# Performance work log

Hardware: AMD Instinct MI355X
Metric: run time of the kernel (lower is better)

## Reference

```python
import jax, jax.numpy as jnp
import numpy as np
import math

D_MODEL = 768
H = 12
B = 2
N = 2048


def _layernorm(x, w, b, eps=1e-5):
    mu = jnp.mean(x, axis=-1, keepdims=True)
    var = jnp.var(x, axis=-1, keepdims=True)
    return (x - mu) / jnp.sqrt(var + eps) * w + b


def _mha(q, k, v, h):
    # q,k,v: [B,N,D] -> [B,h,N,dk]
    Bq, Nq, D = q.shape
    dk = D // h
    q = q.reshape(Bq, Nq, h, dk).transpose(0, 2, 1, 3)
    k = k.reshape(Bq, Nq, h, dk).transpose(0, 2, 1, 3)
    v = v.reshape(Bq, Nq, h, dk).transpose(0, 2, 1, 3)
    att = jnp.einsum('bhnd,bhmd->bhnm', q, k) / math.sqrt(dk)
    att = jax.nn.softmax(att, axis=-1)
    out = jnp.einsum('bhnm,bhmd->bhnd', att, v)
    return out.transpose(0, 2, 1, 3).reshape(Bq, Nq, D)


def setup_inputs() -> dict:
    key = jax.random.key(0)
    ks = jax.random.split(key, 12)
    d = D_MODEL
    w = lambda k: jax.random.normal(k, (d, d), jnp.float32) * 0.001
    inp = {
        'rgb': jax.random.normal(ks[0], (B, N, d), jnp.float32),
        'ir': jax.random.normal(ks[1], (B, N, d), jnp.float32),
        'ln0_w': jnp.ones((d,), jnp.float32), 'ln0_b': jnp.zeros((d,), jnp.float32),
        'ln1_w': jnp.ones((d,), jnp.float32), 'ln1_b': jnp.zeros((d,), jnp.float32),
        'Wq_vis': w(ks[2]), 'bq_vis': jnp.zeros((d,), jnp.float32),
        'Wk_vis': w(ks[3]), 'bk_vis': jnp.zeros((d,), jnp.float32),
        'Wq_ir': w(ks[4]), 'bq_ir': jnp.zeros((d,), jnp.float32),
        'Wk_ir': w(ks[5]), 'bk_ir': jnp.zeros((d,), jnp.float32),
        'Wv_vis': w(ks[6]), 'bv_vis': jnp.zeros((d,), jnp.float32),
        'Wv_ir': w(ks[7]), 'bv_ir': jnp.zeros((d,), jnp.float32),
        'Wo_vis': w(ks[8]), 'bo_vis': jnp.zeros((d,), jnp.float32),
        'Wo_ir': w(ks[9]), 'bo_ir': jnp.zeros((d,), jnp.float32),
    }
    return inp


def reference(rgb, ir, ln0_w, ln0_b, ln1_w, ln1_b,
              Wq_vis, bq_vis, Wk_vis, bk_vis, Wq_ir, bq_ir, Wk_ir, bk_ir,
              Wv_vis, bv_vis, Wv_ir, bv_ir, Wo_vis, bo_vis, Wo_ir, bo_ir):
    rgb_n = _layernorm(rgb, ln0_w, ln0_b)
    ir_n = _layernorm(ir, ln1_w, ln1_b)
    q_vis = rgb_n @ Wq_vis + bq_vis
    k_vis = rgb_n @ Wk_vis + bk_vis
    q_ir = ir_n @ Wq_ir + bq_ir
    k_ir = ir_n @ Wk_ir + bk_ir
    v_vis = rgb_n @ Wv_vis + bv_vis
    v_ir = ir_n @ Wv_ir + bv_ir
    out_vis = _mha(q_ir, k_vis, v_vis, H) @ Wo_vis + bo_vis
    out_ir = _mha(q_vis, k_ir, v_ir, H) @ Wo_ir + bo_ir
    return (out_vis, out_ir)
```

## Files before the change

kernel.cpp:

```cpp
#include <hip/hip_runtime.h>
#include <stdint.h>

#define NTOK 4096
#define DM   768

typedef unsigned short u16;
typedef __attribute__((ext_vector_type(8))) short bf16x8;
typedef __attribute__((ext_vector_type(4))) float f32x4;

__device__ __forceinline__ u16 f2bf(float f){
  union { float f; unsigned u; } x; x.f = f;
  return (u16)((x.u + 0x7fffu + ((x.u >> 16) & 1u)) >> 16);
}
__device__ __forceinline__ unsigned fbits(float f){
  union { float f; unsigned u; } x; x.f = f; return x.u;
}
__device__ __forceinline__ int invk(int t){
  return (((t>>3)&1)<<4) | (((t>>2)&1)<<3) | (((t>>4)&1)<<2) | (t&3);
}

__device__ __forceinline__ void dma16(u16* lds, const u16* g){
  __builtin_amdgcn_global_load_lds(
      (const __attribute__((address_space(1))) unsigned*)g,
      (__attribute__((address_space(3))) unsigned*)lds, 16, 0, 0);
}

struct PreArgs {
  const float* wsrc[8]; u16* wdst[8];
  const float* rgb; const float* ir;
  const float* w0; const float* b0; const float* w1; const float* b1;
  u16* rgbn; u16* irn;
};

__global__ __launch_bounds__(256) void k_pre(PreArgs a){
  __shared__ float T[64][65];
  __shared__ float red[8];
  int bid = blockIdx.x;
  int t = threadIdx.x;
  if (bid < 1152){
    int z = bid / 144, r = bid % 144;
    int k0 = (r % 12) * 64, n0 = (r / 12) * 64;
    const float* W = a.wsrc[z];
    u16* Wt = a.wdst[z];
    int rr = t >> 4, c4 = (t & 15) * 4;
    #pragma unroll
    for (int it = 0; it < 4; ++it){
      int row = rr + it * 16;
      float4 v = *(const float4*)(W + (size_t)(k0 + row) * DM + n0 + c4);
      T[row][c4+0] = v.x; T[row][c4+1] = v.y; T[row][c4+2] = v.z; T[row][c4+3] = v.w;
    }
    __syncthreads();
    #pragma unroll
    for (int it = 0; it < 4; ++it){
      int row = rr + it * 16;
      union { u16 us[4]; uint2 u2; } pk;
      #pragma unroll
      for (int i = 0; i < 4; i++) pk.us[i] = f2bf(T[c4+i][row]);
      *(uint2*)(Wt + (size_t)(n0 + row) * DM + k0 + c4) = pk.u2;
    }
  } else {
    int row = bid - 1152;
    const float *src, *w, *b; u16* dst;
    if (row < NTOK){ src = a.rgb + (size_t)row * DM; w = a.w0; b = a.b0; dst = a.rgbn + (size_t)row * DM; }
    else { int r2 = row - NTOK; src = a.ir + (size_t)r2 * DM; w = a.w1; b = a.b1; dst = a.irn + (size_t)r2 * DM; }
    float v0 = src[t], v1 = src[t+256], v2 = src[t+512];
    float s = v0+v1+v2, ss = v0*v0 + v1*v1 + v2*v2;
    #pragma unroll
    for (int m = 1; m < 64; m <<= 1){ s += __shfl_xor(s, m, 64); ss += __shfl_xor(ss, m, 64); }
    int wv = t >> 6;
    if ((t & 63) == 0){ red[wv] = s; red[4+wv] = ss; }
    __syncthreads();
    s  = red[0]+red[1]+red[2]+red[3];
    ss = red[4]+red[5]+red[6]+red[7];
    float mu   = s * (1.f/768.f);
    float var  = ss * (1.f/768.f) - mu*mu;
    float rstd = rsqrtf(var + 1e-5f);
    dst[t]     = f2bf((v0-mu)*rstd*w[t]     + b[t]);
    dst[t+256] = f2bf((v1-mu)*rstd*w[t+256] + b[t+256]);
    dst[t+512] = f2bf((v2-mu)*rstd*w[t+512] + b[t+512]);
  }
}

struct MmArgs { const u16* A[6]; const u16* Bm[6]; const float* bias[6]; void* out[6]; float scale[6]; int mode[6]; };

__global__ __launch_bounds__(256) void k_mm(MmArgs g){
  __shared__ u16 As[2][128*32];
  __shared__ u16 Bs[2][128*32];
  int z = blockIdx.z;
  int mode = g.mode[z];
  const u16* A = g.A[z];
  const u16* B = g.Bm[z];
  const float* bias = g.bias[z];
  float sc = g.scale[z];
  int bx = blockIdx.x;
  int m0, n0;
  if (mode == 2){ m0 = (bx % 6) * 128; n0 = (bx / 6) * 128; }
  else          { m0 = (bx & 31) * 128; n0 = (bx >> 5) * 128; }
  int t = threadIdx.x, lane = t & 63, w = t >> 6, l15 = lane & 15, quad = lane >> 4;
  int wm = (w >> 1) * 64, wn = (w & 1) * 64;
  int lr = lane >> 2, ls = lane & 3;
  int gseg = ls ^ (lr & 3) ^ ((lr >> 2) & 3);
  const u16* Ab = A + (size_t)(m0 + lr) * DM + gseg * 8;
  const u16* Bb = B + (size_t)(n0 + lr) * DM + gseg * 8;
  f32x4 acc[4][4] = {};
  auto stage = [&](int kt, int bufi){
    int k0 = kt * 32;
    #pragma unroll
    for (int c = 0; c < 2; c++){
      int gq = w * 2 + c;
      dma16(&As[bufi][gq*16*32], Ab + (size_t)gq*16*DM + k0);
      dma16(&Bs[bufi][gq*16*32], Bb + (size_t)gq*16*DM + k0);
    }
  };
  stage(0, 0);
  for (int kt = 0; kt < 24; ++kt){
    int cb = kt & 1;
    __syncthreads();
    if (kt + 1 < 24) stage(kt + 1, cb ^ 1);
    bf16x8 af[4], bfr[4];
    #pragma unroll
    for (int i = 0; i < 4; i++){
      int row = wm + i*16 + l15;
      int sg = quad ^ (row & 3) ^ ((row >> 2) & 3);
      af[i] = *(const bf16x8*)&As[cb][row*32 + sg*8];
    }
    #pragma unroll
    for (int j = 0; j < 4; j++){
      int row = wn + j*16 + l15;
      int sg = quad ^ (row & 3) ^ ((row >> 2) & 3);
      bfr[j] = *(const bf16x8*)&Bs[cb][row*32 + sg*8];
    }
    #pragma unroll
    for (int i = 0; i < 4; i++)
      #pragma unroll
      for (int j = 0; j < 4; j++)
        acc[i][j] = __builtin_amdgcn_mfma_f32_16x16x32_bf16(af[i], bfr[j], acc[i][j], 0, 0, 0);
  }
  if (mode == 2){
    #pragma unroll
    for (int i = 0; i < 4; i++)
      #pragma unroll
      for (int j = 0; j < 4; j++){
        int colt = n0 + wn + j*16 + l15;
        int pc = (colt & ~31) | invk(colt & 31);
        #pragma unroll
        for (int r = 0; r < 4; r++){
          int row = m0 + wm + i*16 + quad*4 + r;
          ((u16*)g.out[z])[(size_t)row*4096 + pc] = f2bf((acc[i][j][r] + bias[row]) * sc);
        }
      }
  } else {
    #pragma unroll
    for (int i = 0; i < 4; i++)
      #pragma unroll
      for (int j = 0; j < 4; j++){
        int col = n0 + wn + j*16 + l15;
        float bc = bias[col];
        #pragma unroll
        for (int r = 0; r < 4; r++){
          int row = m0 + wm + i*16 + quad*4 + r;
          float v = (acc[i][j][r] + bc) * sc;
          if (mode == 1) ((float*)g.out[z])[(size_t)row*DM + col] = v;
          else           ((u16*) g.out[z])[(size_t)row*DM + col] = f2bf(v);
        }
      }
  }
}

struct AttnArgs { const u16* q[2]; const u16* k[2]; const u16* vT[2]; u16* o[2]; };

__global__ __launch_bounds__(256, 4) void k_attn(AttnArgs a){
  __shared__ u16 Kb[2][64*64];
  __shared__ u16 Vb[2][64*64];
  int qt = blockIdx.x, bh = blockIdx.y, aid = blockIdx.z;
  int b = bh / 12, h = bh % 12;
  const u16* Q  = a.q[aid]  + (size_t)b*2048*DM + h*64;
  const u16* K  = a.k[aid]  + (size_t)b*2048*DM + h*64;
  const u16* VT = a.vT[aid] + (size_t)h*64*NTOK + (size_t)b*2048;
  u16* O = a.o[aid] + (size_t)b*2048*DM + h*64;
  int t = threadIdx.x, lane = t & 63, w = t >> 6, l15 = lane & 15, quad = lane >> 4;
  bf16x8 aq[2][2];
  #pragma unroll
  for (int i = 0; i < 2; i++)
    #pragma unroll
    for (int hf = 0; hf < 2; hf++)
      aq[i][hf] = *(const bf16x8*)(Q + (size_t)(qt*128 + w*32 + i*16 + l15)*DM + hf*32 + quad*8);
  f32x4 oacc[2][4] = {};
  float psum[2] = {0.f, 0.f};
  int lr = lane >> 3, ls = lane & 7;
  int gsw = ls ^ lr;
  const u16* Kbase = K  + (size_t)lr*DM   + gsw*8;
  const u16* Vbase = VT + (size_t)lr*NTOK + gsw*8;
  auto stage = [&](int kt, int bufi){
    #pragma unroll
    for (int c = 0; c < 2; c++){
      int g = c*4 + w;
      dma16(&Kb[bufi][g*8*64], Kbase + (size_t)(kt*64 + g*8)*DM);
      dma16(&Vb[bufi][g*8*64], Vbase + (size_t)(g*8)*NTOK + kt*64);
    }
  };
  stage(0, 0);
  for (int kt = 0; kt < 32; ++kt){
    int cb = kt & 1;
    __syncthreads();
    if (kt < 31) stage(kt + 1, cb ^ 1);
    bf16x8 kf[4][2], vf[4][2];
    #pragma unroll
    for (int j = 0; j < 4; j++){
      int row = j*16 + l15, sw = row & 7;
      #pragma unroll
      for (int hf = 0; hf < 2; hf++){
        kf[j][hf] = *(const bf16x8*)&Kb[cb][row*64 + ((hf*4 + quad) ^ sw)*8];
        vf[j][hf] = *(const bf16x8*)&Vb[cb][row*64 + ((hf*4 + quad) ^ sw)*8];
      }
    }
    #pragma unroll
    for (int i = 0; i < 2; i++){
      f32x4 st[4];
      #pragma unroll
      for (int j = 0; j < 4; j++){
        f32x4 s = {0.f, 0.f, 0.f, 0.f};
        s = __builtin_amdgcn_mfma_f32_16x16x32_bf16(kf[j][0], aq[i][0], s, 0, 0, 0);
        s = __builtin_amdgcn_mfma_f32_16x16x32_bf16(kf[j][1], aq[i][1], s, 0, 0, 0);
        st[j] = s;
      }
      f32x4 pe[4];
      #pragma unroll
      for (int j = 0; j < 4; j++){
        #pragma unroll
        for (int r = 0; r < 4; r++) pe[j][r] = __builtin_amdgcn_exp2f(st[j][r]);
        psum[i] += (pe[j][0] + pe[j][1]) + (pe[j][2] + pe[j][3]);
      }
      #pragma unroll
      for (int h2 = 0; h2 < 2; h2++){
        union { uint4 u; bf16x8 v; } pf;
        pf.u.x = __builtin_amdgcn_perm(fbits(pe[2*h2][1]),   fbits(pe[2*h2][0]),   0x07060302u);
        pf.u.y = __builtin_amdgcn_perm(fbits(pe[2*h2][3]),   fbits(pe[2*h2][2]),   0x07060302u);
        pf.u.z = __builtin_amdgcn_perm(fbits(pe[2*h2+1][1]), fbits(pe[2*h2+1][0]), 0x07060302u);
        pf.u.w = __builtin_amdgcn_perm(fbits(pe[2*h2+1][3]), fbits(pe[2*h2+1][2]), 0x07060302u);
        #pragma unroll
        for (int j = 0; j < 4; j++)
          oacc[i][j] = __builtin_amdgcn_mfma_f32_16x16x32_bf16(vf[j][h2], pf.v, oacc[i][j], 0, 0, 0);
      }
    }
  }
  #pragma unroll
  for (int i = 0; i < 2; i++){
    float s = psum[i];
    s += __shfl_xor(s, 16, 64);
    s += __shfl_xor(s, 32, 64);
    float oinv = 1.f / s;
    int token = qt*128 + w*32 + i*16 + l15;
    #pragma unroll
    for (int j = 0; j < 4; j++){
      float v0 = oacc[i][j][0] * oinv, v1 = oacc[i][j][1] * oinv;
      float v2 = oacc[i][j][2] * oinv, v3 = oacc[i][j][3] * oinv;
      uint2 pk;
      pk.x = (unsigned)f2bf(v0) | ((unsigned)f2bf(v1) << 16);
      pk.y = (unsigned)f2bf(v2) | ((unsigned)f2bf(v3) << 16);
      *(uint2*)&O[(size_t)token*DM + j*16 + quad*4] = pk;
    }
  }
}

extern "C" void kernel_launch(void* const* d_in, const int* in_sizes, int n_in,
                              void* d_out, int out_size, void* d_ws, size_t ws_size,
                              hipStream_t stream){
  const float* rgb  = (const float*)d_in[0];
  const float* ir   = (const float*)d_in[1];
  const float* ln0w = (const float*)d_in[2];
  const float* ln0b = (const float*)d_in[3];
  const float* ln1w = (const float*)d_in[4];
  const float* ln1b = (const float*)d_in[5];
  const float* Wq_vis = (const float*)d_in[6];  const float* bq_vis = (const float*)d_in[7];
  const float* Wk_vis = (const float*)d_in[8];  const float* bk_vis = (const float*)d_in[9];
  const float* Wq_ir  = (const float*)d_in[10]; const float* bq_ir  = (const float*)d_in[11];
  const float* Wk_ir  = (const float*)d_in[12]; const float* bk_ir  = (const float*)d_in[13];
  const float* Wv_vis = (const float*)d_in[14]; const float* bv_vis = (const float*)d_in[15];
  const float* Wv_ir  = (const float*)d_in[16]; const float* bv_ir  = (const float*)d_in[17];
  const float* Wo_vis = (const float*)d_in[18]; const float* bo_vis = (const float*)d_in[19];
  const float* Wo_ir  = (const float*)d_in[20]; const float* bo_ir  = (const float*)d_in[21];
  float* out = (float*)d_out;

  char* ws = (char*)d_ws;
  size_t off = 0;
  auto alloc = [&](size_t bytes)->void*{
    void* p = ws + off; off += (bytes + 255) & ~(size_t)255; return p;
  };
  const size_t MAT = (size_t)NTOK * DM;
  u16* Wt[8];
  for (int i = 0; i < 8; i++) Wt[i] = (u16*)alloc((size_t)DM * DM * 2);
  u16* rgbn = (u16*)alloc(MAT*2);
  u16* irn  = (u16*)alloc(MAT*2);
  u16* qv = (u16*)alloc(MAT*2); u16* kv = (u16*)alloc(MAT*2);
  u16* qi = (u16*)alloc(MAT*2); u16* ki = (u16*)alloc(MAT*2);
  u16* tv  = (u16*)alloc(MAT*2);
  u16* ti  = (u16*)alloc(MAT*2);
  u16* at0 = (u16*)alloc(MAT*2);
  u16* at1 = (u16*)alloc(MAT*2);

  PreArgs pa;
  const float* wsrc[8] = {Wq_vis, Wk_vis, Wv_vis, Wq_ir, Wk_ir, Wv_ir, Wo_vis, Wo_ir};
  for (int i = 0; i < 8; i++){ pa.wsrc[i] = wsrc[i]; pa.wdst[i] = Wt[i]; }
  pa.rgb = rgb; pa.ir = ir; pa.w0 = ln0w; pa.b0 = ln0b; pa.w1 = ln1w; pa.b1 = ln1b;
  pa.rgbn = rgbn; pa.irn = irn;
  k_pre<<<dim3(1152 + 2*NTOK), 256, 0, stream>>>(pa);

  const float QS = 0.125f * 1.44269504088896f;
  MmArgs gp = {};
  gp.A[0]=rgbn; gp.Bm[0]=Wt[0]; gp.bias[0]=bq_vis; gp.out[0]=qv; gp.scale[0]=QS;  gp.mode[0]=0;
  gp.A[1]=rgbn; gp.Bm[1]=Wt[1]; gp.bias[1]=bk_vis; gp.out[1]=kv; gp.scale[1]=1.f; gp.mode[1]=0;
  gp.A[2]=irn;  gp.Bm[2]=Wt[3]; gp.bias[2]=bq_ir;  gp.out[2]=qi; gp.scale[2]=QS;  gp.mode[2]=0;
  gp.A[3]=irn;  gp.Bm[3]=Wt[4]; gp.bias[3]=bk_ir;  gp.out[3]=ki; gp.scale[3]=1.f; gp.mode[3]=0;
  gp.A[4]=Wt[2]; gp.Bm[4]=rgbn; gp.bias[4]=bv_vis; gp.out[4]=tv; gp.scale[4]=1.f; gp.mode[4]=2;
  gp.A[5]=Wt[5]; gp.Bm[5]=irn;  gp.bias[5]=bv_ir;  gp.out[5]=ti; gp.scale[5]=1.f; gp.mode[5]=2;
  k_mm<<<dim3(192,1,6), 256, 0, stream>>>(gp);

  AttnArgs aa;
  aa.q[0]=qi; aa.k[0]=kv; aa.vT[0]=tv; aa.o[0]=at0;
  aa.q[1]=qv; aa.k[1]=ki; aa.vT[1]=ti; aa.o[1]=at1;
  k_attn<<<dim3(16,24,2), 256, 0, stream>>>(aa);

  MmArgs gf = {};
  gf.A[0]=at0; gf.Bm[0]=Wt[6]; gf.bias[0]=bo_vis; gf.out[0]=out;       gf.scale[0]=1.f; gf.mode[0]=1;
  gf.A[1]=at1; gf.Bm[1]=Wt[7]; gf.bias[1]=bo_ir;  gf.out[1]=out + MAT; gf.scale[1]=1.f; gf.mode[1]=1;
  k_mm<<<dim3(192,1,2), 256, 0, stream>>>(gf);
}
```

Before: 266.0 us.

## Use two-wave attention blocks with 64 queries per wave; warp-per-row layernorm

```diff
diff --git a/kernel.cpp b/kernel.cpp
--- a/kernel.cpp
+++ b/kernel.cpp
@@ -34,7 +34,6 @@
 
 __global__ __launch_bounds__(256) void k_pre(PreArgs a){
   __shared__ float T[64][65];
-  __shared__ float red[8];
   int bid = blockIdx.x;
   int t = threadIdx.x;
   if (bid < 1152){
@@ -59,25 +58,37 @@
       *(uint2*)(Wt + (size_t)(n0 + row) * DM + k0 + c4) = pk.u2;
     }
   } else {
-    int row = bid - 1152;
+    int row = (bid - 1152) * 4 + (t >> 6);
+    int lane = t & 63;
     const float *src, *w, *b; u16* dst;
     if (row < NTOK){ src = a.rgb + (size_t)row * DM; w = a.w0; b = a.b0; dst = a.rgbn + (size_t)row * DM; }
     else { int r2 = row - NTOK; src = a.ir + (size_t)r2 * DM; w = a.w1; b = a.b1; dst = a.irn + (size_t)r2 * DM; }
-    float v0 = src[t], v1 = src[t+256], v2 = src[t+512];
-    float s = v0+v1+v2, ss = v0*v0 + v1*v1 + v2*v2;
+    float4 v[3];
+    float s = 0.f, ss = 0.f;
+    #pragma unroll
+    for (int p = 0; p < 3; p++){
+      v[p] = *(const float4*)(src + lane*4 + p*256);
+      s  += (v[p].x + v[p].y) + (v[p].z + v[p].w);
+      ss += (v[p].x*v[p].x + v[p].y*v[p].y) + (v[p].z*v[p].z + v[p].w*v[p].w);
+    }
     #pragma unroll
     for (int m = 1; m < 64; m <<= 1){ s += __shfl_xor(s, m, 64); ss += __shfl_xor(ss, m, 64); }
-    int wv = t >> 6;
-    if ((t & 63) == 0){ red[wv] = s; red[4+wv] = ss; }
-    __syncthreads();
-    s  = red[0]+red[1]+red[2]+red[3];
-    ss = red[4]+red[5]+red[6]+red[7];
     float mu   = s * (1.f/768.f);
     float var  = ss * (1.f/768.f) - mu*mu;
     float rstd = rsqrtf(var + 1e-5f);
-    dst[t]     = f2bf((v0-mu)*rstd*w[t]     + b[t]);
-    dst[t+256] = f2bf((v1-mu)*rstd*w[t+256] + b[t+256]);
-    dst[t+512] = f2bf((v2-mu)*rstd*w[t+512] + b[t+512]);
+    #pragma unroll
+    for (int p = 0; p < 3; p++){
+      float4 w4 = *(const float4*)(w + lane*4 + p*256);
+      float4 b4 = *(const float4*)(b + lane*4 + p*256);
+      float o0 = (v[p].x-mu)*rstd*w4.x + b4.x;
+      float o1 = (v[p].y-mu)*rstd*w4.y + b4.y;
+      float o2 = (v[p].z-mu)*rstd*w4.z + b4.z;
+      float o3 = (v[p].w-mu)*rstd*w4.w + b4.w;
+      uint2 pk;
+      pk.x = (unsigned)f2bf(o0) | ((unsigned)f2bf(o1) << 16);
+      pk.y = (unsigned)f2bf(o2) | ((unsigned)f2bf(o3) << 16);
+      *(uint2*)(dst + lane*4 + p*256) = pk;
+    }
   }
 }
 
@@ -169,7 +180,7 @@
 
 struct AttnArgs { const u16* q[2]; const u16* k[2]; const u16* vT[2]; u16* o[2]; };
 
-__global__ __launch_bounds__(256, 4) void k_attn(AttnArgs a){
+__global__ __launch_bounds__(128, 2) void k_attn(AttnArgs a){
   __shared__ u16 Kb[2][64*64];
   __shared__ u16 Vb[2][64*64];
   int qt = blockIdx.x, bh = blockIdx.y, aid = blockIdx.z;
@@ -179,22 +190,22 @@
   const u16* VT = a.vT[aid] + (size_t)h*64*NTOK + (size_t)b*2048;
   u16* O = a.o[aid] + (size_t)b*2048*DM + h*64;
   int t = threadIdx.x, lane = t & 63, w = t >> 6, l15 = lane & 15, quad = lane >> 4;
-  bf16x8 aq[2][2];
+  bf16x8 aq[4][2];
   #pragma unroll
-  for (int i = 0; i < 2; i++)
+  for (int i = 0; i < 4; i++)
     #pragma unroll
     for (int hf = 0; hf < 2; hf++)
-      aq[i][hf] = *(const bf16x8*)(Q + (size_t)(qt*128 + w*32 + i*16 + l15)*DM + hf*32 + quad*8);
-  f32x4 oacc[2][4] = {};
-  float psum[2] = {0.f, 0.f};
+      aq[i][hf] = *(const bf16x8*)(Q + (size_t)(qt*128 + w*64 + i*16 + l15)*DM + hf*32 + quad*8);
+  f32x4 oacc[4][4] = {};
+  float psum[4] = {0.f, 0.f, 0.f, 0.f};
   int lr = lane >> 3, ls = lane & 7;
   int gsw = ls ^ lr;
   const u16* Kbase = K  + (size_t)lr*DM   + gsw*8;
   const u16* Vbase = VT + (size_t)lr*NTOK + gsw*8;
   auto stage = [&](int kt, int bufi){
     #pragma unroll
-    for (int c = 0; c < 2; c++){
-      int g = c*4 + w;
+    for (int c = 0; c < 4; c++){
+      int g = w*4 + c;
       dma16(&Kb[bufi][g*8*64], Kbase + (size_t)(kt*64 + g*8)*DM);
       dma16(&Vb[bufi][g*8*64], Vbase + (size_t)(g*8)*NTOK + kt*64);
     }
@@ -215,7 +226,7 @@
       }
     }
     #pragma unroll
-    for (int i = 0; i < 2; i++){
+    for (int i = 0; i < 4; i++){
       f32x4 st[4];
       #pragma unroll
       for (int j = 0; j < 4; j++){
@@ -245,12 +256,12 @@
     }
   }
   #pragma unroll
-  for (int i = 0; i < 2; i++){
+  for (int i = 0; i < 4; i++){
     float s = psum[i];
     s += __shfl_xor(s, 16, 64);
     s += __shfl_xor(s, 32, 64);
     float oinv = 1.f / s;
-    int token = qt*128 + w*32 + i*16 + l15;
+    int token = qt*128 + w*64 + i*16 + l15;
     #pragma unroll
     for (int j = 0; j < 4; j++){
       float v0 = oacc[i][j][0] * oinv, v1 = oacc[i][j][1] * oinv;
@@ -304,7 +315,7 @@
   for (int i = 0; i < 8; i++){ pa.wsrc[i] = wsrc[i]; pa.wdst[i] = Wt[i]; }
   pa.rgb = rgb; pa.ir = ir; pa.w0 = ln0w; pa.b0 = ln0b; pa.w1 = ln1w; pa.b1 = ln1b;
   pa.rgbn = rgbn; pa.irn = irn;
-  k_pre<<<dim3(1152 + 2*NTOK), 256, 0, stream>>>(pa);
+  k_pre<<<dim3(1152 + 2048), 256, 0, stream>>>(pa);
 
   const float QS = 0.125f * 1.44269504088896f;
   MmArgs gp = {};
@@ -319,7 +330,7 @@
   AttnArgs aa;
   aa.q[0]=qi; aa.k[0]=kv; aa.vT[0]=tv; aa.o[0]=at0;
   aa.q[1]=qv; aa.k[1]=ki; aa.vT[1]=ti; aa.o[1]=at1;
-  k_attn<<<dim3(16,24,2), 256, 0, stream>>>(aa);
+  k_attn<<<dim3(16,24,2), 128, 0, stream>>>(aa);
 
   MmArgs gf = {};
   gf.A[0]=at0; gf.Bm[0]=Wt[6]; gf.bias[0]=bo_vis; gf.out[0]=out;       gf.scale[0]=1.f; gf.mode[0]=1;
```

Result: slower. 272.5 us (+2.4%).
